# Kernel optimization log

Hardware: AMD Instinct MI355X
Metric: run time of the kernel (lower is better)

## Reference

```python
import jax, jax.numpy as jnp
import numpy as np

B, L, F = 16, 1080, 2
D = 128          # d_model
NC = 64          # num_cnn_channels
DIN = 256        # expand * d_model
N = 16           # d_state
K = 4            # d_conv
R = 8            # dt_rank = ceil(d_model/16)
OUT = 3
NB = 3           # num_mamba_blocks


def setup_inputs() -> dict:
    key = jax.random.key(0)
    ks = jax.random.split(key, 24)
    nrm = lambda k, shape, s=0.05: (jax.random.normal(k, shape) * s).astype(jnp.float32)
    bn = lambda c: jnp.stack([jnp.ones(c), jnp.zeros(c), jnp.zeros(c), jnp.ones(c)]).astype(jnp.float32)
    return {
        'x': jax.random.normal(ks[0], (B, L, F), dtype=jnp.float32),
        'emb_W': nrm(ks[1], (F, D), 0.5), 'emb_b': jnp.zeros(D, jnp.float32),
        'c3_W': nrm(ks[2], (NC, D, 3)), 'c3_b': jnp.zeros(NC, jnp.float32), 'bn3': bn(NC),
        'c5_W': nrm(ks[3], (NC, D, 5)), 'c5_b': jnp.zeros(NC, jnp.float32), 'bn5': bn(NC),
        'c7_W': nrm(ks[4], (NC, D, 7)), 'c7_b': jnp.zeros(NC, jnp.float32), 'bn7': bn(NC),
        'cf_W': nrm(ks[5], (D, 3 * NC, 1)), 'cf_b': jnp.zeros(D, jnp.float32), 'bnf': bn(D),
        'ln_g': jnp.ones((NB, D), jnp.float32), 'ln_b': jnp.zeros((NB, D), jnp.float32),
        'in_W': nrm(ks[6], (NB, 2 * DIN, D)),
        'mconv_W': nrm(ks[7], (NB, DIN, K), 0.2), 'mconv_b': jnp.zeros((NB, DIN), jnp.float32),
        'xproj_W': nrm(ks[8], (NB, R + 2 * N, DIN)),
        'dt_W': nrm(ks[9], (NB, DIN, R), 0.1), 'dt_b': jnp.full((NB, DIN), -1.0, jnp.float32),
        'A_log': jnp.tile(jnp.log(jnp.arange(1.0, N + 1.0, dtype=jnp.float32)), (NB, DIN, 1)),
        'Dp': jnp.ones((NB, DIN), jnp.float32),
        'out_W': nrm(ks[10], (NB, D, DIN)),
        'flin_W': nrm(ks[11], (D, 2 * D)), 'flin_b': jnp.zeros(D, jnp.float32),
        'fc_W': nrm(ks[12], (OUT, D)), 'fc_b': jnp.zeros(OUT, jnp.float32),
    }


def conv1d(x, W, b, pad):
    # x: (B,C,L), W: (O,C,K)
    y = jax.lax.conv_general_dilated(x, W, (1,), [(pad, pad)],
                                     dimension_numbers=('NCH', 'OIH', 'NCH'))
    return y + b[None, :, None]


def bn_relu(x, bn, eps=1e-5):
    g, b, m, v = bn  # each (C,)
    return jax.nn.relu((x - m[None, :, None]) * (g / jnp.sqrt(v + eps))[None, :, None] + b[None, :, None])


def layernorm(x, g, b, eps=1e-5):
    mu = x.mean(-1, keepdims=True)
    var = ((x - mu) ** 2).mean(-1, keepdims=True)
    return (x - mu) / jnp.sqrt(var + eps) * g + b


def pos_encoding(seq_len, d_model):
    pos = jnp.arange(seq_len, dtype=jnp.float32)[:, None]
    div = jnp.exp(jnp.arange(0, d_model, 2, dtype=jnp.float32) * (-np.log(10000.0) / d_model))
    pe = jnp.zeros((seq_len, d_model), jnp.float32)
    pe = pe.at[:, 0::2].set(jnp.sin(pos * div)).at[:, 1::2].set(jnp.cos(pos * div))
    return pe


def selective_scan(u, dt, A, Bm, Cm, Dp):
    # u,dt: (b,l,d); A: (d,n); Bm,Cm: (b,l,n); Dp: (d,)
    dA = jnp.exp(dt[..., None] * A)                    # (b,l,d,n)
    dBu = (dt * u)[..., None] * Bm[:, :, None, :]      # (b,l,d,n)

    def step(h, t):
        dA_t, dBu_t, C_t = t
        h = dA_t * h + dBu_t                           # (b,d,n)
        return h, jnp.einsum('bdn,bn->bd', h, C_t)

    h0 = jnp.zeros((u.shape[0], u.shape[2], A.shape[1]), u.dtype)
    _, ys = jax.lax.scan(step, h0, (jnp.swapaxes(dA, 0, 1), jnp.swapaxes(dBu, 0, 1), jnp.swapaxes(Cm, 0, 1)))
    return jnp.swapaxes(ys, 0, 1) + u * Dp


def mamba_block(x, in_W, conv_W, conv_b, xproj_W, dt_W, dt_b, A_log, Dp, out_W):
    xz = x @ in_W.T                                    # (b,l,2*din)
    xs, z = jnp.split(xz, 2, axis=-1)
    xc = jnp.swapaxes(xs, 1, 2)                        # (b,din,l)
    xc = jax.lax.conv_general_dilated(xc, conv_W[:, None, :], (1,), [(K - 1, 0)],
                                      dimension_numbers=('NCH', 'OIH', 'NCH'),
                                      feature_group_count=DIN)
    u = jax.nn.silu(jnp.swapaxes(xc + conv_b[None, :, None], 1, 2))  # (b,l,din)
    dbl = u @ xproj_W.T
    dt, Bm, Cm = dbl[..., :R], dbl[..., R:R + N], dbl[..., R + N:]
    dt = jax.nn.softplus(dt @ dt_W.T + dt_b)
    A = -jnp.exp(A_log)
    y = selective_scan(u, dt, A, Bm, Cm, Dp)
    return (y * jax.nn.silu(z)) @ out_W.T


def reference(x, emb_W, emb_b, c3_W, c3_b, bn3, c5_W, c5_b, bn5, c7_W, c7_b, bn7,
              cf_W, cf_b, bnf, ln_g, ln_b, in_W, mconv_W, mconv_b, xproj_W,
              dt_W, dt_b, A_log, Dp, out_W, flin_W, flin_b, fc_W, fc_b):
    xe = x @ emb_W + emb_b + pos_encoding(x.shape[1], emb_W.shape[1])  # (B,L,D)
    ci = jnp.swapaxes(xe, 1, 2)                                        # (B,D,L)
    o3 = bn_relu(conv1d(ci, c3_W, c3_b, 1), bn3)
    o5 = bn_relu(conv1d(ci, c5_W, c5_b, 2), bn5)
    o7 = bn_relu(conv1d(ci, c7_W, c7_b, 3), bn7)
    cc = jnp.concatenate([o3, o5, o7], axis=1)                         # (B,3*NC,L)
    cf = bn_relu(conv1d(cc, cf_W, cf_b, 0), bnf)
    cnn_feat = jnp.swapaxes(cf, 1, 2)                                  # (B,L,D)
    m = xe
    for i in range(NB):  # Sequential(LN, Mamba, Dropout) -- no residual, dropout=eval
        m = mamba_block(layernorm(m, ln_g[i], ln_b[i]), in_W[i], mconv_W[i], mconv_b[i],
                        xproj_W[i], dt_W[i], dt_b[i], A_log[i], Dp[i], out_W[i])
    fused = jax.nn.relu(jnp.concatenate([cnn_feat, m], axis=-1) @ flin_W.T + flin_b)
    pooled = fused.mean(axis=1)                                        # AdaptiveAvgPool1d(1)
    return pooled @ fc_W.T + fc_b
```

## Files before the change

kernel.cpp:

```cpp
#include <hip/hip_runtime.h>
#include <math.h>

#define LSEQ   1080
#define NBATCH 16
#define BLROWS (LSEQ*NBATCH)
#define CHN    27
#define LCH    40

#define LPAD 44
#define LPADB 140

typedef __bf16  bf16x8 __attribute__((ext_vector_type(8)));
typedef float   f32x4  __attribute__((ext_vector_type(4)));
typedef short   short8 __attribute__((ext_vector_type(8)));
typedef short   short4v __attribute__((ext_vector_type(4)));

__device__ __forceinline__ float silu_f(float x) { return x / (1.f + __expf(-x)); }

__device__ __forceinline__ unsigned short f2bf(float f) {
    unsigned int u = __float_as_uint(f);
    u += 0x7fffu + ((u >> 16) & 1u);
    return (unsigned short)(u >> 16);
}
__device__ __forceinline__ float bf2f(unsigned short h) {
    return __uint_as_float(((unsigned int)h) << 16);
}
__device__ __forceinline__ void split_bf(float v, unsigned short& h, unsigned short& l) {
    h = f2bf(v);
    l = f2bf(v - bf2f(h));
}

__global__ __launch_bounds__(256) void embed_kernel(
    const float* __restrict__ x, const float* __restrict__ embW,
    const float* __restrict__ embb, float* __restrict__ xe,
    unsigned short* __restrict__ xeh, unsigned short* __restrict__ xel)
{
    int idx = blockIdx.x * 256 + threadIdx.x;
    if (idx >= BLROWS * 128) return;
    int d = idx & 127;
    int r = idx >> 7;
    int t = r % LSEQ;
    float x0 = x[(size_t)r * 2], x1 = x[(size_t)r * 2 + 1];
    int i2 = d & 126;
    float div = expf((float)i2 * (-9.210340371976184f / 128.f));
    float arg = (float)t * div;
    float pe = (d & 1) ? cosf(arg) : sinf(arg);
    float v = fmaf(x0, embW[d], fmaf(x1, embW[128 + d], embb[d] + pe));
    xe[idx] = v;
    unsigned short h, l;
    split_bf(v, h, l);
    xeh[idx] = h; xel[idx] = l;
}

#define JOB_W192  172032
#define JOB_CF    196608
#define JOB_IN    393216
#define JOB_XP    442368
#define JOB_OT    540672
#define JOB_FL    573440
#define JOB_END   574080
__global__ __launch_bounds__(256) void convw_all(
    const float* __restrict__ c3W, const float* __restrict__ c5W,
    const float* __restrict__ c7W, const float* __restrict__ cfW,
    const float* __restrict__ inW, const float* __restrict__ xpW,
    const float* __restrict__ otW, const float* __restrict__ flW,
    const float* __restrict__ c3b, const float* __restrict__ c5b, const float* __restrict__ c7b,
    const float* __restrict__ bn3, const float* __restrict__ bn5, const float* __restrict__ bn7,
    const float* __restrict__ cfb, const float* __restrict__ bnf,
    unsigned short* __restrict__ w192h, unsigned short* __restrict__ w192l,
    unsigned short* __restrict__ cfh, unsigned short* __restrict__ cfl,
    unsigned short* __restrict__ inh, unsigned short* __restrict__ inl,
    unsigned short* __restrict__ xph, unsigned short* __restrict__ xpl,
    unsigned short* __restrict__ oth, unsigned short* __restrict__ otl,
    unsigned short* __restrict__ flh, unsigned short* __restrict__ fll,
    float* __restrict__ schpack)
{
    int idx = blockIdx.x * 256 + threadIdx.x;
    if (idx >= JOB_END) return;
    float v;
    unsigned short *dh, *dl;
    int off;
    if (idx < JOB_W192) {
        off = idx;
        int n = off / 896, kk = off % 896;
        int slot = kk >> 7, d = kk & 127;
        int br = n >> 6, c = n & 63;
        int KT = 3 + 2 * br, pad = 1 + br;
        int tp = slot - 3 + pad;
        const float* w = (br == 0) ? c3W : (br == 1) ? c5W : c7W;
        v = (tp >= 0 && tp < KT) ? w[((c << 7) + d) * KT + tp] : 0.f;
        dh = w192h; dl = w192l;
    } else if (idx < JOB_CF) {
        off = idx - JOB_W192; v = cfW[off]; dh = cfh; dl = cfl;
    } else if (idx < JOB_IN) {
        off = idx - JOB_CF; v = inW[off]; dh = inh; dl = inl;
    } else if (idx < JOB_XP) {
        off = idx - JOB_IN;
        int k = off & 255, n = (off >> 8) & 63, blk = off >> 14;
        v = (n < 40) ? xpW[((size_t)blk * 40 + n) * 256 + k] : 0.f;
        dh = xph; dl = xpl;
    } else if (idx < JOB_OT) {
        off = idx - JOB_XP; v = otW[off]; dh = oth; dl = otl;
    } else if (idx < JOB_FL) {
        off = idx - JOB_OT; v = flW[off]; dh = flh; dl = fll;
    } else {
        int j = idx - JOB_FL;
        if (j < 384) {
            int col = (j < 192) ? j : j - 192;
            int isSh = j >= 192;
            int br = col >> 6, c = col & 63;
            const float* bn = (br == 0) ? bn3 : (br == 1) ? bn5 : bn7;
            float bias = ((br == 0) ? c3b : (br == 1) ? c5b : c7b)[c];
            float g = bn[c], bb = bn[64 + c], m = bn[128 + c], vv = bn[192 + c];
            float scale = g * rsqrtf(vv + 1e-5f);
            float shift = (bias - m) * scale + bb;
            schpack[j] = isSh ? shift : scale;
        } else {
            int j2 = j - 384;
            int col = j2 & 127;
            int isSh = j2 >= 128;
            float g = bnf[col], bb = bnf[128 + col], m = bnf[256 + col], vv = bnf[384 + col];
            float scale = g * rsqrtf(vv + 1e-5f);
            float shift = (cfb[col] - m) * scale + bb;
            schpack[384 + j2] = isSh ? shift : scale;
        }
        return;
    }
    unsigned short h, l;
    split_bf(v, h, l);
    dh[off] = h; dl[off] = l;
}

__global__ __launch_bounds__(256) void gemm_conv(
    const unsigned short* __restrict__ Xh, const unsigned short* __restrict__ Xl,
    const unsigned short* __restrict__ Wh, const unsigned short* __restrict__ Wl,
    const float* __restrict__ sc, const float* __restrict__ sh,
    unsigned short* __restrict__ Ch, unsigned short* __restrict__ Cl)
{
    __shared__ unsigned short Ah[70][LPAD], Al[70][LPAD];
    __shared__ unsigned short Bh[64][LPADB], Bl[64][LPADB];
    const int tid = threadIdx.x;
    const int n0 = blockIdx.x * 64, t0 = blockIdx.y * 64, b = blockIdx.z;
    const size_t boff = (size_t)b * LSEQ;
    const int lane = tid & 63, wid = tid >> 6;
    const int wr = wid >> 1, wc = wid & 1;
    const int fr = lane & 15, fq = lane >> 4;
    const short8 zz = {0, 0, 0, 0, 0, 0, 0, 0};
    f32x4 acc[2][2];
#pragma unroll
    for (int m = 0; m < 2; ++m)
#pragma unroll
        for (int n = 0; n < 2; ++n) acc[m][n] = (f32x4){0.f, 0.f, 0.f, 0.f};

    for (int ks = 0; ks < 128; ks += 32) {
#pragma unroll
        for (int l = 0; l < 2; ++l) {
            int c = tid + l * 256;
            if (c < 280) {
                int row = c >> 2, kc = (c & 3) << 3;
                int ts = t0 - 3 + row;
                short8 vh = zz, vl = zz;
                if (ts >= 0 && ts < LSEQ) {
                    size_t s = (boff + ts) * 128 + ks + kc;
                    vh = *(const short8*)&Xh[s];
                    vl = *(const short8*)&Xl[s];
                }
                *(short8*)&Ah[row][kc] = vh;
                *(short8*)&Al[row][kc] = vl;
            }
        }
        for (int g = 0; g < 2; ++g) {
            const int ntap = (g == 0) ? 4 : 3;
#pragma unroll
            for (int l = 0; l < 4; ++l) {
                int c = tid + l * 256;
                int col = c >> 4, rem = c & 15, tt = rem >> 2, kq = (rem & 3) << 3;
                if (tt < ntap) {
                    int tap = g * 4 + tt;
                    size_t s = (size_t)(n0 + col) * 896 + tap * 128 + ks + kq;
                    *(short8*)&Bh[col][tt * 32 + kq] = *(const short8*)&Wh[s];
                    *(short8*)&Bl[col][tt * 32 + kq] = *(const short8*)&Wl[s];
                }
            }
            __syncthreads();
            for (int tt = 0; tt < ntap; ++tt) {
                int tap = g * 4 + tt;
                bf16x8 bhf[2], blf[2];
#pragma unroll
                for (int n = 0; n < 2; ++n) {
                    int col = wc * 32 + n * 16 + fr;
                    bhf[n] = __builtin_bit_cast(bf16x8, *(const short8*)&Bh[col][tt * 32 + fq * 8]);
                    blf[n] = __builtin_bit_cast(bf16x8, *(const short8*)&Bl[col][tt * 32 + fq * 8]);
                }
#pragma unroll
                for (int m = 0; m < 2; ++m) {
                    int rowA = wr * 32 + m * 16 + fr + tap;
                    bf16x8 ahf = __builtin_bit_cast(bf16x8, *(const short8*)&Ah[rowA][fq * 8]);
                    bf16x8 alf = __builtin_bit_cast(bf16x8, *(const short8*)&Al[rowA][fq * 8]);
#pragma unroll
                    for (int n = 0; n < 2; ++n) {
                        acc[m][n] = __builtin_amdgcn_mfma_f32_16x16x32_bf16(ahf, bhf[n], acc[m][n], 0, 0, 0);
                        acc[m][n] = __builtin_amdgcn_mfma_f32_16x16x32_bf16(ahf, blf[n], acc[m][n], 0, 0, 0);
                        acc[m][n] = __builtin_amdgcn_mfma_f32_16x16x32_bf16(alf, bhf[n], acc[m][n], 0, 0, 0);
                    }
                }
            }
            __syncthreads();
        }
    }
    unsigned short* Chb = Ch + (size_t)b * LSEQ * 192;
    unsigned short* Clb = Cl + (size_t)b * LSEQ * 192;
#pragma unroll
    for (int m = 0; m < 2; ++m) {
#pragma unroll
        for (int n = 0; n < 2; ++n) {
            int colg = n0 + wc * 32 + n * 16 + fr;
            float scl = sc[colg], shf2 = sh[colg];
#pragma unroll
            for (int r = 0; r < 4; ++r) {
                int t = t0 + wr * 32 + m * 16 + fq * 4 + r;
                if (t >= LSEQ) continue;
                float v = fmaf(acc[m][n][r], scl, shf2);
                v = v > 0.f ? v : 0.f;
                unsigned short h, l;
                split_bf(v, h, l);
                Chb[(size_t)t * 192 + colg] = h;
                Clb[(size_t)t * 192 + colg] = l;
            }
        }
    }
}

template<int BM, int BN>
__global__ __launch_bounds__(256) void gemm_plain(
    const unsigned short* __restrict__ Aph, const unsigned short* __restrict__ Apl, int lda,
    const unsigned short* __restrict__ Wh, const unsigned short* __restrict__ Wl, int Kd,
    int Ntot, int epi,
    const float* __restrict__ sc, const float* __restrict__ sh, const float* __restrict__ bias,
    float* __restrict__ Cf, int ldc,
    unsigned short* __restrict__ Ch, unsigned short* __restrict__ Cl, int ldch)
{
    constexpr int WM = BM / 2, WN = BN / 2;
    constexpr int MR = WM / 16, NR = WN / 16;
    constexpr int ACH = (BM * 4) / 256;
    constexpr int BCH = (BN * 4) / 256;
    __shared__ unsigned short Ah[BM][LPAD], Al[BM][LPAD];
    __shared__ unsigned short Bh[BN][LPAD], Bl[BN][LPAD];
    const int tid = threadIdx.x;
    const int b = blockIdx.z, t0 = blockIdx.y * BM, n0 = blockIdx.x * BN;
    const unsigned short* Abh = Aph + (size_t)b * LSEQ * lda;
    const unsigned short* Abl = Apl + (size_t)b * LSEQ * lda;
    const int lane = tid & 63, wid = tid >> 6;
    const int wr = wid >> 1, wc = wid & 1;
    const int fr = lane & 15, fq = lane >> 4;
    f32x4 acc[MR][NR];
#pragma unroll
    for (int m = 0; m < MR; ++m)
#pragma unroll
        for (int n = 0; n < NR; ++n) acc[m][n] = (f32x4){0.f, 0.f, 0.f, 0.f};

    const short8 zz = {0, 0, 0, 0, 0, 0, 0, 0};
    for (int ks = 0; ks < Kd; ks += 32) {
#pragma unroll
        for (int l = 0; l < ACH; ++l) {
            int c = tid + l * 256;
            int row = c >> 2, kc = (c & 3) << 3;
            int t = t0 + row;
            short8 vh = zz, vl = zz;
            if (t < LSEQ) {
                size_t s = (size_t)t * lda + ks + kc;
                vh = *(const short8*)&Abh[s];
                vl = *(const short8*)&Abl[s];
            }
            *(short8*)&Ah[row][kc] = vh;
            *(short8*)&Al[row][kc] = vl;
        }
#pragma unroll
        for (int l = 0; l < BCH; ++l) {
            int c = tid + l * 256;
            int col = c >> 2, kc = (c & 3) << 3;
            size_t s = (size_t)(n0 + col) * Kd + ks + kc;
            *(short8*)&Bh[col][kc] = *(const short8*)&Wh[s];
            *(short8*)&Bl[col][kc] = *(const short8*)&Wl[s];
        }
        __syncthreads();
        bf16x8 bhf[NR], blf[NR];
#pragma unroll
        for (int n = 0; n < NR; ++n) {
            int col = wc * WN + n * 16 + fr;
            bhf[n] = __builtin_bit_cast(bf16x8, *(const short8*)&Bh[col][fq * 8]);
            blf[n] = __builtin_bit_cast(bf16x8, *(const short8*)&Bl[col][fq * 8]);
        }
#pragma unroll
        for (int m = 0; m < MR; ++m) {
            int rowr = wr * WM + m * 16 + fr;
            bf16x8 ahf = __builtin_bit_cast(bf16x8, *(const short8*)&Ah[rowr][fq * 8]);
            bf16x8 alf = __builtin_bit_cast(bf16x8, *(const short8*)&Al[rowr][fq * 8]);
#pragma unroll
            for (int n = 0; n < NR; ++n) {
                acc[m][n] = __builtin_amdgcn_mfma_f32_16x16x32_bf16(ahf, bhf[n], acc[m][n], 0, 0, 0);
                acc[m][n] = __builtin_amdgcn_mfma_f32_16x16x32_bf16(ahf, blf[n], acc[m][n], 0, 0, 0);
                acc[m][n] = __builtin_amdgcn_mfma_f32_16x16x32_bf16(alf, bhf[n], acc[m][n], 0, 0, 0);
            }
        }
        __syncthreads();
    }

    float* Cfb = Cf ? Cf + (size_t)b * LSEQ * ldc : nullptr;
    unsigned short* Chb = Ch ? Ch + (size_t)b * LSEQ * ldch : nullptr;
    unsigned short* Clb = Cl ? Cl + (size_t)b * LSEQ * ldch : nullptr;

    if (epi == 4) {
        float* red = reinterpret_cast<float*>(&Ah[0][0]);
        float part[MR][4], mu[MR][4], rs[MR][4];
#pragma unroll
        for (int m = 0; m < MR; ++m)
#pragma unroll
            for (int r = 0; r < 4; ++r) {
                float p = 0.f;
#pragma unroll
                for (int n = 0; n < NR; ++n) p += acc[m][n][r];
#pragma unroll
                for (int o2 = 1; o2 < 16; o2 <<= 1) p += __shfl_xor(p, o2, 64);
                part[m][r] = p;
            }
        if (fr == 0) {
#pragma unroll
            for (int m = 0; m < MR; ++m)
#pragma unroll
                for (int r = 0; r < 4; ++r)
                    red[(wr * 32 + m * 16 + fq * 4 + r) * 2 + wc] = part[m][r];
        }
        __syncthreads();
#pragma unroll
        for (int m = 0; m < MR; ++m)
#pragma unroll
            for (int r = 0; r < 4; ++r) {
                int row = wr * 32 + m * 16 + fq * 4 + r;
                mu[m][r] = (red[row * 2] + red[row * 2 + 1]) * (1.f / 128.f);
            }
        __syncthreads();
#pragma unroll
        for (int m = 0; m < MR; ++m)
#pragma unroll
            for (int r = 0; r < 4; ++r) {
                float p = 0.f;
#pragma unroll
                for (int n = 0; n < NR; ++n) {
                    float dv = acc[m][n][r] - mu[m][r];
                    p = fmaf(dv, dv, p);
                }
#pragma unroll
                for (int o2 = 1; o2 < 16; o2 <<= 1) p += __shfl_xor(p, o2, 64);
                part[m][r] = p;
            }
        if (fr == 0) {
#pragma unroll
            for (int m = 0; m < MR; ++m)
#pragma unroll
                for (int r = 0; r < 4; ++r)
                    red[(wr * 32 + m * 16 + fq * 4 + r) * 2 + wc] = part[m][r];
        }
        __syncthreads();
#pragma unroll
        for (int m = 0; m < MR; ++m)
#pragma unroll
            for (int r = 0; r < 4; ++r) {
                int row = wr * 32 + m * 16 + fq * 4 + r;
                rs[m][r] = rsqrtf((red[row * 2] + red[row * 2 + 1]) * (1.f / 128.f) + 1e-5f);
            }
#pragma unroll
        for (int m = 0; m < MR; ++m) {
#pragma unroll
            for (int n = 0; n < NR; ++n) {
                int colg = wc * WN + n * 16 + fr;
                float g = sc[colg], b2 = sh[colg];
#pragma unroll
                for (int r = 0; r < 4; ++r) {
                    int t = t0 + wr * WM + m * 16 + fq * 4 + r;
                    if (t >= LSEQ) continue;
                    float v = (acc[m][n][r] - mu[m][r]) * rs[m][r] * g + b2;
                    unsigned short h, l;
                    split_bf(v, h, l);
                    Chb[(size_t)t * ldch + colg] = h;
                    Clb[(size_t)t * ldch + colg] = l;
                }
            }
        }
        return;
    }

#pragma unroll
    for (int m = 0; m < MR; ++m) {
#pragma unroll
        for (int n = 0; n < NR; ++n) {
            int colg = n0 + wc * WN + n * 16 + fr;
            if (colg >= Ntot) continue;
#pragma unroll
            for (int r = 0; r < 4; ++r) {
                int t = t0 + wr * WM + m * 16 + fq * 4 + r;
                if (t >= LSEQ) continue;
                float v = acc[m][n][r];
                if (epi == 0) {
                    Cfb[(size_t)t * ldc + colg] = v;
                } else if (epi == 1) {
                    v = fmaf(v, sc[colg], sh[colg]);
                    v = v > 0.f ? v : 0.f;
                    unsigned short h, l;
                    split_bf(v, h, l);
                    Chb[(size_t)t * ldch + colg] = h;
                    Clb[(size_t)t * ldch + colg] = l;
                } else if (epi == 2) {
                    v += bias[colg];
                    v = v > 0.f ? v : 0.f;
                    Cfb[(size_t)t * ldc + colg] = v;
                } else {
                    unsigned short h, l;
                    split_bf(v, h, l);
                    Chb[(size_t)t * ldch + colg] = h;
                    Clb[(size_t)t * ldch + colg] = l;
                }
            }
        }
    }
}

__global__ __launch_bounds__(256) void ln_kernel(
    const float* __restrict__ in, const float* __restrict__ g,
    const float* __restrict__ b2, unsigned short* __restrict__ oh,
    unsigned short* __restrict__ ol)
{
    int lane = threadIdx.x & 63;
    int wid  = threadIdx.x >> 6;
    int row = blockIdx.x * 4 + wid;
    if (row >= BLROWS) return;
    const float* rp = in + (size_t)row * 128;
    float v0 = rp[lane], v1 = rp[lane + 64];
    float s = v0 + v1;
#pragma unroll
    for (int o2 = 32; o2 > 0; o2 >>= 1) s += __shfl_xor(s, o2, 64);
    float mu = s * (1.f / 128.f);
    float d0 = v0 - mu, d1 = v1 - mu;
    float q = d0 * d0 + d1 * d1;
#pragma unroll
    for (int o2 = 32; o2 > 0; o2 >>= 1) q += __shfl_xor(q, o2, 64);
    float rs = 1.f / sqrtf(q * (1.f / 128.f) + 1e-5f);
    float y0 = d0 * rs * g[lane]      + b2[lane];
    float y1 = d1 * rs * g[lane + 64] + b2[lane + 64];
    unsigned short h, l;
    size_t o = (size_t)row * 128;
    split_bf(y0, h, l); oh[o + lane] = h;      ol[o + lane] = l;
    split_bf(y1, h, l); oh[o + lane + 64] = h; ol[o + lane + 64] = l;
}

__global__ __launch_bounds__(256) void mconv_kernel(
    const float* __restrict__ xz, const float* __restrict__ Wc,
    const float* __restrict__ bc, float* __restrict__ u,
    unsigned short* __restrict__ uh, unsigned short* __restrict__ ul)
{
    int idx = blockIdx.x * 256 + threadIdx.x;
    int c = idx & 255;
    int r = idx >> 8;
    if (r >= BLROWS) return;
    int t = r % LSEQ;
    const float* xs = xz + (size_t)r * 512 + c;
    float acc = bc[c];
    if (t >= 3) acc = fmaf(xs[-3 * 512], Wc[c * 4 + 0], acc);
    if (t >= 2) acc = fmaf(xs[-2 * 512], Wc[c * 4 + 1], acc);
    if (t >= 1) acc = fmaf(xs[-1 * 512], Wc[c * 4 + 2], acc);
    acc = fmaf(xs[0], Wc[c * 4 + 3], acc);
    float uv = silu_f(acc);
    size_t o = (size_t)r * 256 + c;
    u[o] = uv;
    unsigned short h, l;
    split_bf(uv, h, l);
    uh[o] = h; ul[o] = l;
}

__global__ __launch_bounds__(256) void dtk_kernel(
    const float* __restrict__ dbl, const float* __restrict__ dtW,
    const float* __restrict__ dtb, float* __restrict__ dtout)
{
    int idx = blockIdx.x * 256 + threadIdx.x;
    int c = idx & 255;
    int r = idx >> 8;
    if (r >= BLROWS) return;
    const float* dr = dbl + (size_t)r * 40;
    float a = dtb[c];
#pragma unroll
    for (int j = 0; j < 8; ++j) a = fmaf(dr[j], dtW[c * 8 + j], a);
    float sp = (a > 20.f) ? a : log1pf(__expf(a));
    dtout[(size_t)r * 256 + c] = sp;
}

__global__ __launch_bounds__(256) void scan1_kernel(
    const float* __restrict__ dt, const float* __restrict__ u,
    const float* __restrict__ dbl, const float* __restrict__ Alog,
    float* __restrict__ P, float* __restrict__ S)
{
    __shared__ float sdt[40][64], su[40][64], sB[40][16];
    int bid = blockIdx.x;
    int dg = bid & 3;
    int rest = bid >> 2;
    int ch = rest % CHN;
    int b  = rest / CHN;
    int tid = threadIdx.x;
    int ng = tid & 3, di = tid >> 2;
    int d0 = dg * 64, d = d0 + di, n0 = ng * 4;
    int r0 = b * LSEQ + ch * LCH;
#pragma unroll
    for (int l = 0; l < 3; ++l) {
        int j = tid + l * 256;
        if (j < 640) {
            int row = j >> 4, q = (j & 15) << 2;
            size_t s = (size_t)(r0 + row) * 256 + d0 + q;
            *(float4*)&sdt[row][q] = *(const float4*)&dt[s];
            *(float4*)&su [row][q] = *(const float4*)&u [s];
        }
    }
    if (tid < 160) {
        int row = tid >> 2, q = (tid & 3) << 2;
        *(float4*)&sB[row][q] = *(const float4*)&dbl[(size_t)(r0 + row) * 40 + 8 + q];
    }
    float A2[4];
#pragma unroll
    for (int j = 0; j < 4; ++j) A2[j] = -__expf(Alog[d * 16 + n0 + j]);
    float p[4] = {1.f, 1.f, 1.f, 1.f}, s[4] = {0.f, 0.f, 0.f, 0.f};
    __syncthreads();
#pragma unroll 4
    for (int qi = 0; qi < LCH; ++qi) {
        float dtv = sdt[qi][di];
        float dtu = dtv * su[qi][di];
        float4 Br = *(const float4*)&sB[qi][n0];
        float bv[4] = {Br.x, Br.y, Br.z, Br.w};
#pragma unroll
        for (int j = 0; j < 4; ++j) {
            float a = __expf(dtv * A2[j]);
            p[j] *= a;
            s[j] = fmaf(a, s[j], dtu * bv[j]);
        }
    }
    size_t ob = ((size_t)(b * CHN + ch) * 256 + d) * 16 + n0;
    *(float4*)&P[ob] = make_float4(p[0], p[1], p[2], p[3]);
    *(float4*)&S[ob] = make_float4(s[0], s[1], s[2], s[3]);
}

__global__ __launch_bounds__(256) void scan2_kernel(
    const float* __restrict__ P, const float* __restrict__ S, float* __restrict__ H0)
{
    int idx = blockIdx.x * 256 + threadIdx.x;
    int n = idx & 15;
    int d = (idx >> 4) & 255;
    int b = idx >> 12;
    float h = 0.f;
    for (int ch = 0; ch < CHN; ++ch) {
        size_t o = ((size_t)(b * CHN + ch) * 256 + d) * 16 + n;
        H0[o] = h;
        h = fmaf(P[o], h, S[o]);
    }
}

__global__ __launch_bounds__(256) void scan3_kernel(
    const float* __restrict__ dt, const float* __restrict__ u,
    const float* __restrict__ dbl, const float* __restrict__ Alog,
    const float* __restrict__ H0, const float* __restrict__ Dp,
    const float* __restrict__ xz, unsigned short* __restrict__ gh,
    unsigned short* __restrict__ gl)
{
    __shared__ float sdt[40][64], su[40][64], sz[40][64], sB[40][16], sC[40][16];
    int bid = blockIdx.x;
    int dg = bid & 3;
    int rest = bid >> 2;
    int ch = rest % CHN;
    int b  = rest / CHN;
    int tid = threadIdx.x;
    int ng = tid & 3, di = tid >> 2;
    int d0 = dg * 64, d = d0 + di, n0 = ng * 4;
    int r0 = b * LSEQ + ch * LCH;
#pragma unroll
    for (int l = 0; l < 3; ++l) {
        int j = tid + l * 256;
        if (j < 640) {
            int row = j >> 4, q = (j & 15) << 2;
            size_t s = (size_t)(r0 + row) * 256 + d0 + q;
            *(float4*)&sdt[row][q] = *(const float4*)&dt[s];
            *(float4*)&su [row][q] = *(const float4*)&u [s];
            *(float4*)&sz [row][q] = *(const float4*)&xz[(size_t)(r0 + row) * 512 + 256 + d0 + q];
        }
    }
    if (tid < 160) {
        int row = tid >> 2, q = (tid & 3) << 2;
        *(float4*)&sB[row][q] = *(const float4*)&dbl[(size_t)(r0 + row) * 40 + 8 + q];
        *(float4*)&sC[row][q] = *(const float4*)&dbl[(size_t)(r0 + row) * 40 + 24 + q];
    }
    float A2[4];
#pragma unroll
    for (int j = 0; j < 4; ++j) A2[j] = -__expf(Alog[d * 16 + n0 + j]);
    size_t ob = ((size_t)(b * CHN + ch) * 256 + d) * 16 + n0;
    float4 h4 = *(const float4*)&H0[ob];
    float h[4] = {h4.x, h4.y, h4.z, h4.w};
    float Dpd = Dp[d];
    __syncthreads();
    for (int qi = 0; qi < LCH; ++qi) {
        float dtv = sdt[qi][di];
        float uv  = su[qi][di];
        float dtu = dtv * uv;
        float4 Br = *(const float4*)&sB[qi][n0];
        float4 Cr = *(const float4*)&sC[qi][n0];
        float bv[4] = {Br.x, Br.y, Br.z, Br.w};
        float cv[4] = {Cr.x, Cr.y, Cr.z, Cr.w};
        float pacc = 0.f;
#pragma unroll
        for (int j = 0; j < 4; ++j) {
            float a = __expf(dtv * A2[j]);
            h[j] = fmaf(a, h[j], dtu * bv[j]);
            pacc = fmaf(h[j], cv[j], pacc);
        }
        float acc = pacc + __shfl_xor(pacc, 1);
        acc += __shfl_xor(acc, 2);
        float yv = fmaf(uv, Dpd, acc);
        float gv = yv * silu_f(sz[qi][di]);
        if (ng == 0) sz[qi][di] = gv;
    }
    __syncthreads();
#pragma unroll
    for (int l = 0; l < 3; ++l) {
        int j = tid + l * 256;
        if (j < 640) {
            int row = j >> 4, q = (j & 15) << 2;
            float4 gv4 = *(const float4*)&sz[row][q];
            float gv[4] = {gv4.x, gv4.y, gv4.z, gv4.w};
            alignas(8) unsigned short hs[4], ls[4];
#pragma unroll
            for (int jj = 0; jj < 4; ++jj) split_bf(gv[jj], hs[jj], ls[jj]);
            size_t o = (size_t)(r0 + row) * 256 + d0 + q;
            *(short4v*)&gh[o] = *(short4v*)hs;
            *(short4v*)&gl[o] = *(short4v*)ls;
        }
    }
}

__global__ __launch_bounds__(128) void pool1_kernel(
    const float* __restrict__ fused, float* __restrict__ part)
{
    int d = threadIdx.x;
    int blk = blockIdx.x;
    int ch = blk % CHN;
    int b  = blk / CHN;
    int t0 = ch * LCH;
    float s = 0.f;
    for (int q = 0; q < LCH; ++q)
        s += fused[((size_t)(b * LSEQ + t0 + q)) * 128 + d];
    part[(size_t)(b * CHN + ch) * 128 + d] = s;
}

__global__ __launch_bounds__(128) void pool2_kernel(
    const float* __restrict__ part, const float* __restrict__ fcW,
    const float* __restrict__ fcb, float* __restrict__ out)
{
    __shared__ float pl[128];
    int d = threadIdx.x;
    int b = blockIdx.x;
    float s = 0.f;
    for (int ch = 0; ch < CHN; ++ch) s += part[(size_t)(b * CHN + ch) * 128 + d];
    pl[d] = s * (1.f / 1080.f);
    __syncthreads();
    if (d < 3) {
        float a = fcb[d];
        for (int dd = 0; dd < 128; ++dd) a = fmaf(pl[dd], fcW[d * 128 + dd], a);
        out[b * 3 + d] = a;
    }
}

extern "C" void kernel_launch(void* const* d_in, const int* in_sizes, int n_in,
                              void* d_out, int out_size, void* d_ws, size_t ws_size,
                              hipStream_t stream)
{
    const float* x    = (const float*)d_in[0];
    const float* embW = (const float*)d_in[1];
    const float* embb = (const float*)d_in[2];
    const float* c3W  = (const float*)d_in[3];
    const float* c3b  = (const float*)d_in[4];
    const float* bn3  = (const float*)d_in[5];
    const float* c5W  = (const float*)d_in[6];
    const float* c5b  = (const float*)d_in[7];
    const float* bn5  = (const float*)d_in[8];
    const float* c7W  = (const float*)d_in[9];
    const float* c7b  = (const float*)d_in[10];
    const float* bn7  = (const float*)d_in[11];
    const float* cfW  = (const float*)d_in[12];
    const float* cfb  = (const float*)d_in[13];
    const float* bnf  = (const float*)d_in[14];
    const float* lng  = (const float*)d_in[15];
    const float* lnb  = (const float*)d_in[16];
    const float* inW  = (const float*)d_in[17];
    const float* mcW  = (const float*)d_in[18];
    const float* mcb  = (const float*)d_in[19];
    const float* xpW  = (const float*)d_in[20];
    const float* dtW  = (const float*)d_in[21];
    const float* dtbp = (const float*)d_in[22];
    const float* Alog = (const float*)d_in[23];
    const float* Dp   = (const float*)d_in[24];
    const float* outW = (const float*)d_in[25];
    const float* flW  = (const float*)d_in[26];
    const float* flb  = (const float*)d_in[27];
    const float* fcW  = (const float*)d_in[28];
    const float* fcb  = (const float*)d_in[29];

    float* ws = (float*)d_ws;
    size_t off = 0;
    auto alloc = [&](size_t n) { float* p = ws + off; off += n; return p; };
    float* xe   = alloc((size_t)BLROWS * 128);
    float* xz   = alloc((size_t)BLROWS * 512);
    float* ub   = alloc((size_t)BLROWS * 256);
    float* dtt  = alloc((size_t)BLROWS * 256);
    float* dbl  = alloc((size_t)BLROWS * 40);
    float* Pb   = alloc((size_t)NBATCH * CHN * 256 * 16);
    float* Sb   = alloc((size_t)NBATCH * CHN * 256 * 16);
    float* h0b  = alloc((size_t)NBATCH * CHN * 256 * 16);
    float* schpack = alloc(640);
    float* fused = xz;

    off = (off + 3) & ~(size_t)3;
    unsigned short* us = (unsigned short*)(ws + off);
    size_t uo = 0;
    auto ualloc = [&](size_t n) { unsigned short* p = us + uo; uo += n; return p; };
    unsigned short* cch  = ualloc((size_t)BLROWS * 192);
    unsigned short* ccl  = ualloc((size_t)BLROWS * 192);
    unsigned short* finh = ualloc((size_t)BLROWS * 256);
    unsigned short* finl = ualloc((size_t)BLROWS * 256);
    unsigned short* ubh  = ualloc((size_t)BLROWS * 256);
    unsigned short* ubl  = ualloc((size_t)BLROWS * 256);
    unsigned short* xeh  = ualloc((size_t)BLROWS * 128);
    unsigned short* xel  = ualloc((size_t)BLROWS * 128);
    unsigned short* w192h = ualloc((size_t)192 * 896); unsigned short* w192l = ualloc((size_t)192 * 896);
    unsigned short* cfh = ualloc(128 * 192); unsigned short* cfl = ualloc(128 * 192);
    unsigned short* inh = ualloc((size_t)1536 * 128); unsigned short* inl = ualloc((size_t)1536 * 128);
    unsigned short* xph = ualloc((size_t)3 * 64 * 256); unsigned short* xpl = ualloc((size_t)3 * 64 * 256);
    unsigned short* oth = ualloc((size_t)384 * 256); unsigned short* otl = ualloc((size_t)384 * 256);
    unsigned short* flh = ualloc((size_t)128 * 256); unsigned short* fll = ualloc((size_t)128 * 256);
    unsigned short* lnxh = cch;
    unsigned short* lnxl = ccl;
    unsigned short* gbh  = ubh;
    unsigned short* gbl  = ubl;
    (void)ws_size; (void)in_sizes; (void)n_in; (void)out_size;

    convw_all<<<(JOB_END + 255) / 256, 256, 0, stream>>>(
        c3W, c5W, c7W, cfW, inW, xpW, outW, flW,
        c3b, c5b, c7b, bn3, bn5, bn7, cfb, bnf,
        w192h, w192l, cfh, cfl, inh, inl, xph, xpl, oth, otl, flh, fll, schpack);

    embed_kernel<<<(BLROWS * 128) / 256, 256, 0, stream>>>(x, embW, embb, xe, xeh, xel);

    dim3 gconv(3, 17, NBATCH);
    gemm_conv<<<gconv, 256, 0, stream>>>(xeh, xel, w192h, w192l, schpack, schpack + 192, cch, ccl);
    dim3 g17(1, 17, NBATCH);
    gemm_plain<64, 128><<<g17, 256, 0, stream>>>(
        cch, ccl, 192, cfh, cfl, 192, 128, 1,
        schpack + 384, schpack + 512, nullptr, nullptr, 0, finh, finl, 256);

    ln_kernel<<<BLROWS / 4, 256, 0, stream>>>(xe, lng, lnb, lnxh, lnxl);

    const int SCAN_BLKS = NBATCH * CHN * 4;
    for (int i = 0; i < 3; ++i) {
        dim3 gin(4, 17, NBATCH);
        gemm_plain<64, 128><<<gin, 256, 0, stream>>>(
            lnxh, lnxl, 128, inh + (size_t)i * 512 * 128, inl + (size_t)i * 512 * 128, 128,
            512, 0, nullptr, nullptr, nullptr, xz, 512, nullptr, nullptr, 0);

        mconv_kernel<<<BLROWS, 256, 0, stream>>>(xz, mcW + i * 256 * 4, mcb + i * 256, ub, ubh, ubl);

        gemm_plain<64, 64><<<g17, 256, 0, stream>>>(
            ubh, ubl, 256, xph + (size_t)i * 64 * 256, xpl + (size_t)i * 64 * 256, 256,
            40, 0, nullptr, nullptr, nullptr, dbl, 40, nullptr, nullptr, 0);

        dtk_kernel<<<BLROWS, 256, 0, stream>>>(dbl, dtW + i * 256 * 8, dtbp + i * 256, dtt);

        scan1_kernel<<<SCAN_BLKS, 256, 0, stream>>>(
            dtt, ub, dbl, Alog + i * 256 * 16, Pb, Sb);
        scan2_kernel<<<(NBATCH * 256 * 16) / 256, 256, 0, stream>>>(Pb, Sb, h0b);
        scan3_kernel<<<SCAN_BLKS, 256, 0, stream>>>(
            dtt, ub, dbl, Alog + i * 256 * 16, h0b, Dp + i * 256, xz, gbh, gbl);

        if (i < 2) {
            gemm_plain<64, 128><<<g17, 256, 0, stream>>>(
                gbh, gbl, 256, oth + (size_t)i * 128 * 256, otl + (size_t)i * 128 * 256, 256,
                128, 4, lng + (i + 1) * 128, lnb + (i + 1) * 128, nullptr,
                nullptr, 0, lnxh, lnxl, 128);
        } else {
            gemm_plain<64, 128><<<g17, 256, 0, stream>>>(
                gbh, gbl, 256, oth + (size_t)i * 128 * 256, otl + (size_t)i * 128 * 256, 256,
                128, 3, nullptr, nullptr, nullptr, nullptr, 0, finh + 128, finl + 128, 256);
        }
    }

    gemm_plain<64, 128><<<g17, 256, 0, stream>>>(
        finh, finl, 256, flh, fll, 256, 128, 2,
        nullptr, nullptr, flb, fused, 128, nullptr, nullptr, 0);

    pool1_kernel<<<NBATCH * CHN, 128, 0, stream>>>(fused, Pb);
    pool2_kernel<<<NBATCH, 128, 0, stream>>>(Pb, fcW, fcb, (float*)d_out);
}
```

Baseline: 649.7 us.

## Fuse Mamba depthwise conv, x_proj GEMM and dt projection into one kernel

Replaces the separate conv+SiLU, x_proj GEMM and dt-projection/softplus kernels with a single tiled kernel. Each block computes conv outputs directly into shared memory as split-bf16 GEMM operands, runs the MFMA x_proj, and then applies the dt projection from shared memory. This removes the intermediate bf16 u buffers and two launches. In exchange, the elementwise work now runs on only a few hundred blocks, with a serial row loop in the dt stage, which reduces parallelism.

```diff
diff --git a/kernel.cpp b/kernel.cpp
--- a/kernel.cpp
+++ b/kernel.cpp
@@ -453,44 +453,119 @@
     split_bf(y1, h, l); oh[o + lane + 64] = h; ol[o + lane + 64] = l;
 }
 
-__global__ __launch_bounds__(256) void mconv_kernel(
+__global__ __launch_bounds__(256) void mxd_kernel(
     const float* __restrict__ xz, const float* __restrict__ Wc,
-    const float* __restrict__ bc, float* __restrict__ u,
-    unsigned short* __restrict__ uh, unsigned short* __restrict__ ul)
-{
-    int idx = blockIdx.x * 256 + threadIdx.x;
-    int c = idx & 255;
-    int r = idx >> 8;
-    if (r >= BLROWS) return;
-    int t = r % LSEQ;
-    const float* xs = xz + (size_t)r * 512 + c;
-    float acc = bc[c];
-    if (t >= 3) acc = fmaf(xs[-3 * 512], Wc[c * 4 + 0], acc);
-    if (t >= 2) acc = fmaf(xs[-2 * 512], Wc[c * 4 + 1], acc);
-    if (t >= 1) acc = fmaf(xs[-1 * 512], Wc[c * 4 + 2], acc);
-    acc = fmaf(xs[0], Wc[c * 4 + 3], acc);
-    float uv = silu_f(acc);
-    size_t o = (size_t)r * 256 + c;
-    u[o] = uv;
-    unsigned short h, l;
-    split_bf(uv, h, l);
-    uh[o] = h; ul[o] = l;
-}
-
-__global__ __launch_bounds__(256) void dtk_kernel(
-    const float* __restrict__ dbl, const float* __restrict__ dtW,
-    const float* __restrict__ dtb, float* __restrict__ dtout)
-{
-    int idx = blockIdx.x * 256 + threadIdx.x;
-    int c = idx & 255;
-    int r = idx >> 8;
-    if (r >= BLROWS) return;
-    const float* dr = dbl + (size_t)r * 40;
-    float a = dtb[c];
-#pragma unroll
-    for (int j = 0; j < 8; ++j) a = fmaf(dr[j], dtW[c * 8 + j], a);
-    float sp = (a > 20.f) ? a : log1pf(__expf(a));
-    dtout[(size_t)r * 256 + c] = sp;
+    const float* __restrict__ bc,
+    const unsigned short* __restrict__ Wh, const unsigned short* __restrict__ Wl,
+    const float* __restrict__ dtW, const float* __restrict__ dtb,
+    float* __restrict__ u, float* __restrict__ dbl, float* __restrict__ dtt)
+{
+    __shared__ unsigned short Ah[64][72], Al[64][72];
+    __shared__ unsigned short Bh[64][72], Bl[64][72];
+    __shared__ float sdbl[64][44];
+    const int tid = threadIdx.x;
+    const int t0 = blockIdx.x * 64, b = blockIdx.y;
+    const size_t rb = (size_t)b * LSEQ;
+    const int lane = tid & 63, wid = tid >> 6;
+    const int wr = wid >> 1, wc2 = wid & 1;
+    const int fr = lane & 15, fq = lane >> 4;
+    f32x4 acc[2][2];
+#pragma unroll
+    for (int m = 0; m < 2; ++m)
+#pragma unroll
+        for (int n = 0; n < 2; ++n) acc[m][n] = (f32x4){0.f, 0.f, 0.f, 0.f};
+
+    for (int ks = 0; ks < 256; ks += 64) {
+#pragma unroll
+        for (int l = 0; l < 16; ++l) {
+            int j = tid + l * 256;
+            int row = j >> 6, cl = j & 63;
+            int c = ks + cl;
+            int t = t0 + row;
+            unsigned short h = 0, lo = 0;
+            if (t < LSEQ) {
+                const float* xs = xz + (rb + t) * 512 + c;
+                float a = bc[c];
+                if (t >= 3) a = fmaf(xs[-3 * 512], Wc[c * 4 + 0], a);
+                if (t >= 2) a = fmaf(xs[-2 * 512], Wc[c * 4 + 1], a);
+                if (t >= 1) a = fmaf(xs[-1 * 512], Wc[c * 4 + 2], a);
+                a = fmaf(xs[0], Wc[c * 4 + 3], a);
+                float uv = silu_f(a);
+                u[(rb + t) * 256 + c] = uv;
+                split_bf(uv, h, lo);
+            }
+            Ah[row][cl] = h;
+            Al[row][cl] = lo;
+        }
+#pragma unroll
+        for (int l = 0; l < 2; ++l) {
+            int j = tid + l * 256;
+            int col = j >> 3, kc = (j & 7) << 3;
+            size_t s = (size_t)col * 256 + ks + kc;
+            *(short8*)&Bh[col][kc] = *(const short8*)&Wh[s];
+            *(short8*)&Bl[col][kc] = *(const short8*)&Wl[s];
+        }
+        __syncthreads();
+#pragma unroll
+        for (int kk = 0; kk < 64; kk += 32) {
+            bf16x8 bhf[2], blf[2];
+#pragma unroll
+            for (int n = 0; n < 2; ++n) {
+                int col = wc2 * 32 + n * 16 + fr;
+                bhf[n] = __builtin_bit_cast(bf16x8, *(const short8*)&Bh[col][kk + fq * 8]);
+                blf[n] = __builtin_bit_cast(bf16x8, *(const short8*)&Bl[col][kk + fq * 8]);
+            }
+#pragma unroll
+            for (int m = 0; m < 2; ++m) {
+                int rowr = wr * 32 + m * 16 + fr;
+                bf16x8 ahf = __builtin_bit_cast(bf16x8, *(const short8*)&Ah[rowr][kk + fq * 8]);
+                bf16x8 alf = __builtin_bit_cast(bf16x8, *(const short8*)&Al[rowr][kk + fq * 8]);
+#pragma unroll
+                for (int n = 0; n < 2; ++n) {
+                    acc[m][n] = __builtin_amdgcn_mfma_f32_16x16x32_bf16(ahf, bhf[n], acc[m][n], 0, 0, 0);
+                    acc[m][n] = __builtin_amdgcn_mfma_f32_16x16x32_bf16(ahf, blf[n], acc[m][n], 0, 0, 0);
+                    acc[m][n] = __builtin_amdgcn_mfma_f32_16x16x32_bf16(alf, bhf[n], acc[m][n], 0, 0, 0);
+                }
+            }
+        }
+        __syncthreads();
+    }
+
+#pragma unroll
+    for (int m = 0; m < 2; ++m) {
+#pragma unroll
+        for (int n = 0; n < 2; ++n) {
+            int colg = wc2 * 32 + n * 16 + fr;
+#pragma unroll
+            for (int r = 0; r < 4; ++r) {
+                int rowl = wr * 32 + m * 16 + fq * 4 + r;
+                int t = t0 + rowl;
+                if (colg < 40) {
+                    sdbl[rowl][colg] = acc[m][n][r];
+                    if (t < LSEQ)
+                        dbl[(rb + t) * 40 + colg] = acc[m][n][r];
+                }
+            }
+        }
+    }
+    __syncthreads();
+    {
+        int c = tid;
+        float w0 = dtW[c * 8 + 0], w1 = dtW[c * 8 + 1], w2 = dtW[c * 8 + 2], w3 = dtW[c * 8 + 3];
+        float w4 = dtW[c * 8 + 4], w5 = dtW[c * 8 + 5], w6 = dtW[c * 8 + 6], w7 = dtW[c * 8 + 7];
+        float bbv = dtb[c];
+        for (int r = 0; r < 64; ++r) {
+            int t = t0 + r;
+            if (t >= LSEQ) break;
+            float a = bbv;
+            a = fmaf(sdbl[r][0], w0, a); a = fmaf(sdbl[r][1], w1, a);
+            a = fmaf(sdbl[r][2], w2, a); a = fmaf(sdbl[r][3], w3, a);
+            a = fmaf(sdbl[r][4], w4, a); a = fmaf(sdbl[r][5], w5, a);
+            a = fmaf(sdbl[r][6], w6, a); a = fmaf(sdbl[r][7], w7, a);
+            float sp = (a > 20.f) ? a : log1pf(__expf(a));
+            dtt[(rb + t) * 256 + c] = sp;
+        }
+    }
 }
 
 __global__ __launch_bounds__(256) void scan1_kernel(
@@ -729,8 +804,8 @@
     unsigned short* ccl  = ualloc((size_t)BLROWS * 192);
     unsigned short* finh = ualloc((size_t)BLROWS * 256);
     unsigned short* finl = ualloc((size_t)BLROWS * 256);
-    unsigned short* ubh  = ualloc((size_t)BLROWS * 256);
-    unsigned short* ubl  = ualloc((size_t)BLROWS * 256);
+    unsigned short* gbh  = ualloc((size_t)BLROWS * 256);
+    unsigned short* gbl  = ualloc((size_t)BLROWS * 256);
     unsigned short* xeh  = ualloc((size_t)BLROWS * 128);
     unsigned short* xel  = ualloc((size_t)BLROWS * 128);
     unsigned short* w192h = ualloc((size_t)192 * 896); unsigned short* w192l = ualloc((size_t)192 * 896);
@@ -741,8 +816,6 @@
     unsigned short* flh = ualloc((size_t)128 * 256); unsigned short* fll = ualloc((size_t)128 * 256);
     unsigned short* lnxh = cch;
     unsigned short* lnxl = ccl;
-    unsigned short* gbh  = ubh;
-    unsigned short* gbl  = ubl;
     (void)ws_size; (void)in_sizes; (void)n_in; (void)out_size;
 
     convw_all<<<(JOB_END + 255) / 256, 256, 0, stream>>>(
@@ -768,13 +841,12 @@
             lnxh, lnxl, 128, inh + (size_t)i * 512 * 128, inl + (size_t)i * 512 * 128, 128,
             512, 0, nullptr, nullptr, nullptr, xz, 512, nullptr, nullptr, 0);
 
-        mconv_kernel<<<BLROWS, 256, 0, stream>>>(xz, mcW + i * 256 * 4, mcb + i * 256, ub, ubh, ubl);
-
-        gemm_plain<64, 64><<<g17, 256, 0, stream>>>(
-            ubh, ubl, 256, xph + (size_t)i * 64 * 256, xpl + (size_t)i * 64 * 256, 256,
-            40, 0, nullptr, nullptr, nullptr, dbl, 40, nullptr, nullptr, 0);
-
-        dtk_kernel<<<BLROWS, 256, 0, stream>>>(dbl, dtW + i * 256 * 8, dtbp + i * 256, dtt);
+        dim3 gmxd(17, NBATCH);
+        mxd_kernel<<<gmxd, 256, 0, stream>>>(
+            xz, mcW + i * 256 * 4, mcb + i * 256,
+            xph + (size_t)i * 64 * 256, xpl + (size_t)i * 64 * 256,
+            dtW + i * 256 * 8, dtbp + i * 256,
+            ub, dbl, dtt);
 
         scan1_kernel<<<SCAN_BLKS, 256, 0, stream>>>(
             dtt, ub, dbl, Alog + i * 256 * 16, Pb, Sb);
```

Measured after the change: 831.2 us. 1.28x slower.
